# Kernel tuning notes

Measured on AMD Instinct MI355X. Metric: run time of the kernel, lower is better.

Reference implementation:

```python
import jax, jax.numpy as jnp
import numpy as np

N = 2048      # nodes per graph
Q = 9         # output_dim (emotion nodes)
D = 256       # input_dim == hidden_dim
L = 4         # num_layers - 1 GIN layers
B = 32        # batch
E = 32768     # edges per graph
EPS = 1e-5    # BatchNorm eps


def _bn(x, g, b, m, v):
    # eval-mode BatchNorm1d over last (channel) dim
    return (x - m) * (g * jax.lax.rsqrt(v + EPS)) + b


def setup_inputs() -> dict:
    key = jax.random.key(0)
    ks = jax.random.split(key, 18)
    s = 1.0 / np.sqrt(D)
    return {
        "batch_feature": jax.random.normal(ks[0], (B, N, D), jnp.float32),
        "edge_mat": jax.random.randint(ks[1], (2, E), 0, N, dtype=jnp.int32),
        "emotion_emb": jax.random.normal(ks[2], (1, Q, D), jnp.float32) * 0.05,
        "mlp_w1": jax.random.normal(ks[3], (L, D, D), jnp.float32) * s,
        "mlp_b1": jnp.zeros((L, D), jnp.float32),
        "mlp_bn_g": jnp.ones((L, D), jnp.float32),
        "mlp_bn_b": jnp.zeros((L, D), jnp.float32),
        "mlp_bn_m": jax.random.normal(ks[4], (L, D), jnp.float32) * 0.1,
        "mlp_bn_v": jax.random.uniform(ks[5], (L, D), jnp.float32, 0.5, 1.5),
        "mlp_w2": jax.random.normal(ks[6], (L, D, D), jnp.float32) * s,
        "mlp_b2": jnp.zeros((L, D), jnp.float32),
        "bn_g": jnp.ones((L, D), jnp.float32),
        "bn_b": jnp.zeros((L, D), jnp.float32),
        "bn_m": jax.random.normal(ks[7], (L, D), jnp.float32) * 0.1,
        "bn_v": jax.random.uniform(ks[8], (L, D), jnp.float32, 0.5, 1.5),
        "pred_w": jax.random.normal(ks[9], (L + 1, D), jnp.float32) * s,
        "pred_b": jnp.zeros((L + 1,), jnp.float32),
    }


def reference(batch_feature, edge_mat, emotion_emb, mlp_w1, mlp_b1,
              mlp_bn_g, mlp_bn_b, mlp_bn_m, mlp_bn_v, mlp_w2, mlp_b2,
              bn_g, bn_b, bn_m, bn_v, pred_w, pred_b):
    # overwrite first Q node rows with shared emotion embeddings
    h = batch_feature.at[:, :Q, :].set(emotion_emb)          # [B, N, D]
    src, dst = edge_mat[0], edge_mat[1]

    def spmm(x):
        # Adj @ x with self-loops; graph topology shared across batch.
        gathered = x[:, dst, :]                              # [B, E, D]
        agg = jax.vmap(
            lambda g: jax.ops.segment_sum(g, src, num_segments=N)
        )(gathered)                                          # [B, N, D]
        return agg + x  # self-loop (identity added to adjacency)

    hidden = [h]
    for l in range(L):
        pooled = spmm(h)
        # 2-layer GIN MLP: Linear -> BN -> ReLU -> Linear
        t = jnp.einsum('bnd,de->bne', pooled, mlp_w1[l]) + mlp_b1[l]
        t = jax.nn.relu(_bn(t, mlp_bn_g[l], mlp_bn_b[l], mlp_bn_m[l], mlp_bn_v[l]))
        t = jnp.einsum('bnd,de->bne', t, mlp_w2[l]) + mlp_b2[l]
        # outer BatchNorm + ReLU
        h = jax.nn.relu(_bn(t, bn_g[l], bn_b[l], bn_m[l], bn_v[l]))
        hidden.append(h)

    score = jnp.zeros((B, Q), jnp.float32)
    for l, hl in enumerate(hidden):
        h_emotion = hl[:, :Q, :]                             # [B, Q, D]
        score = score + jnp.einsum('bqd,d->bq', h_emotion, pred_w[l]) + pred_b[l]
    return jax.nn.sigmoid(score)                             # [B, Q]
```

## Files before the change

### kernel.cpp

```cpp
#include <hip/hip_runtime.h>
#include <hip/hip_bf16.h>

#define NN 2048
#define QQ 9
#define DD 256
#define LL 4
#define BB 32
#define EE 32768
#define EPSV 1e-5f

typedef __attribute__((ext_vector_type(8))) short bf16x8;
typedef __attribute__((ext_vector_type(8))) ushort u16x8;
typedef __attribute__((ext_vector_type(4))) float f32x4;
typedef __attribute__((ext_vector_type(4))) int i32x4;

__device__ __forceinline__ ushort f2bf(float x)
{
    uint u = __float_as_uint(x);
    u += 0x7FFFu + ((u >> 16) & 1u);
    return (ushort)(u >> 16);
}
__device__ __forceinline__ float bf2f(ushort h)
{
    return __uint_as_float(((uint)h) << 16);
}

__device__ __forceinline__ void gload16(const ushort* g, ushort* l)
{
    __builtin_amdgcn_global_load_lds(
        (const __attribute__((address_space(1))) void*)g,
        (__attribute__((address_space(3))) void*)l, 16, 0, 0);
}

__global__ void k_count(const int* __restrict__ src, int* __restrict__ cnt)
{
    int e = blockIdx.x * blockDim.x + threadIdx.x;
    if (e < EE) atomicAdd(&cnt[src[e]], 1);
}

__global__ __launch_bounds__(256) void k_scan(const int* __restrict__ cnt,
                                              int* __restrict__ row_ptr,
                                              int* __restrict__ cursor)
{
    __shared__ int part[256];
    int t = threadIdx.x;
    int local[8];
    int s = 0;
    #pragma unroll
    for (int i = 0; i < 8; ++i) { local[i] = cnt[t * 8 + i]; s += local[i]; }
    part[t] = s;
    __syncthreads();
    for (int off = 1; off < 256; off <<= 1) {
        int v = (t >= off) ? part[t - off] : 0;
        __syncthreads();
        part[t] += v;
        __syncthreads();
    }
    int run = part[t] - s;
    #pragma unroll
    for (int i = 0; i < 8; ++i) {
        int idx = t * 8 + i;
        row_ptr[idx] = run;
        cursor[idx]  = run;
        run += local[i];
    }
    if (t == 255) row_ptr[NN] = run;
}

__global__ void k_fill(const int* __restrict__ src, const int* __restrict__ dst,
                       int* __restrict__ cursor, int* __restrict__ col)
{
    int e = blockIdx.x * blockDim.x + threadIdx.x;
    if (e < EE) {
        int p = atomicAdd(&cursor[src[e]], 1);
        col[p] = dst[e];
    }
}

__global__ void k_prep0(const float4* __restrict__ bf, const float4* __restrict__ emo,
                        ushort4* __restrict__ hhi)
{
    int total = BB * NN * (DD / 4);
    for (int idx = blockIdx.x * blockDim.x + threadIdx.x; idx < total;
         idx += gridDim.x * blockDim.x) {
        int d4 = idx & 63;
        int n  = (idx >> 6) & (NN - 1);
        float4 v = (n < QQ) ? emo[n * 64 + d4] : bf[idx];
        ushort4 h;
        h.x = f2bf(v.x); h.y = f2bf(v.y); h.z = f2bf(v.z); h.w = f2bf(v.w);
        hhi[idx] = h;
    }
}

__global__ __launch_bounds__(256) void k_spmm6(
    const ushort* __restrict__ phi,
    const int* __restrict__ row_ptr, const int* __restrict__ col,
    ushort* __restrict__ ohi)
{
    int x     = blockIdx.x & 7;
    int local = blockIdx.x >> 3;
    int w     = threadIdx.x >> 6;
    int t     = threadIdx.x & 63;
    int inst  = local * 4 + w;
    int pl    = inst >> 11;
    int n     = inst & (NN - 1);
    int b     = x * 4 + pl * 2 + (t >> 5);
    int q     = t & 31;
    const ushort* base = phi + (size_t)b * NN * DD + q * 8;

    u16x8 sv = *(const u16x8*)(base + (size_t)n * DD);
    float a[8];
    #pragma unroll
    for (int k = 0; k < 8; ++k) a[k] = bf2f((ushort)sv[k]);

    int beg = row_ptr[n], end = row_ptr[n + 1];
    int j = beg;
    for (; j < end && (j & 3); ++j) {
        u16x8 g = *(const u16x8*)(base + (size_t)col[j] * DD);
        #pragma unroll
        for (int k = 0; k < 8; ++k) a[k] += bf2f((ushort)g[k]);
    }
    for (; j + 8 <= end; j += 8) {
        i32x4 c0 = *(const i32x4*)(col + j);
        i32x4 c1 = *(const i32x4*)(col + j + 4);
        u16x8 g[8];
        g[0] = *(const u16x8*)(base + (size_t)c0.x * DD);
        g[1] = *(const u16x8*)(base + (size_t)c0.y * DD);
        g[2] = *(const u16x8*)(base + (size_t)c0.z * DD);
        g[3] = *(const u16x8*)(base + (size_t)c0.w * DD);
        g[4] = *(const u16x8*)(base + (size_t)c1.x * DD);
        g[5] = *(const u16x8*)(base + (size_t)c1.y * DD);
        g[6] = *(const u16x8*)(base + (size_t)c1.z * DD);
        g[7] = *(const u16x8*)(base + (size_t)c1.w * DD);
        #pragma unroll
        for (int u = 0; u < 8; ++u)
            #pragma unroll
            for (int k = 0; k < 8; ++k) a[k] += bf2f((ushort)g[u][k]);
    }
    if (j + 4 <= end) {
        i32x4 c = *(const i32x4*)(col + j);
        u16x8 g[4];
        g[0] = *(const u16x8*)(base + (size_t)c.x * DD);
        g[1] = *(const u16x8*)(base + (size_t)c.y * DD);
        g[2] = *(const u16x8*)(base + (size_t)c.z * DD);
        g[3] = *(const u16x8*)(base + (size_t)c.w * DD);
        #pragma unroll
        for (int u = 0; u < 4; ++u)
            #pragma unroll
            for (int k = 0; k < 8; ++k) a[k] += bf2f((ushort)g[u][k]);
        j += 4;
    }
    for (; j < end; ++j) {
        u16x8 g = *(const u16x8*)(base + (size_t)col[j] * DD);
        #pragma unroll
        for (int k = 0; k < 8; ++k) a[k] += bf2f((ushort)g[k]);
    }

    u16x8 o;
    #pragma unroll
    for (int k = 0; k < 8; ++k) o[k] = f2bf(a[k]);
    *(u16x8*)(ohi + ((size_t)b * NN + n) * DD + q * 8) = o;
}

__global__ __launch_bounds__(256) void k_wprep(const float* __restrict__ w1,
                                               const float* __restrict__ w2,
                                               ushort* __restrict__ wt_hi)
{
    __shared__ float tile[32][36];
    int bx = blockIdx.x;
    int mat = bx >> 6;
    int tt  = bx & 63;
    int tk = (tt >> 3) * 32;
    int tn = (tt & 7) * 32;
    const float* src = (mat < 4) ? (w1 + (size_t)mat * DD * DD)
                                 : (w2 + (size_t)(mat - 4) * DD * DD);
    int t = threadIdx.x;
    int r = t >> 3, c0 = (t & 7) * 4;
    float4 v = *(const float4*)(src + (size_t)(tk + r) * DD + tn + c0);
    tile[r][c0 + 0] = v.x; tile[r][c0 + 1] = v.y;
    tile[r][c0 + 2] = v.z; tile[r][c0 + 3] = v.w;
    __syncthreads();
    int nn = t >> 3, kq = (t & 7) * 4;
    ushort4 hh;
    hh.x = f2bf(tile[kq + 0][nn]); hh.y = f2bf(tile[kq + 1][nn]);
    hh.z = f2bf(tile[kq + 2][nn]); hh.w = f2bf(tile[kq + 3][nn]);
    size_t off = (size_t)mat * DD * DD + (size_t)(tn + nn) * DD + tk + kq;
    *(ushort4*)(wt_hi + off) = hh;
}

__global__ __launch_bounds__(256) void k_gemm_fused(
    const ushort* __restrict__ A, const ushort* __restrict__ W1t,
    const ushort* __restrict__ W2t,
    const float* __restrict__ b1, const float* __restrict__ g1,
    const float* __restrict__ be1, const float* __restrict__ m1,
    const float* __restrict__ v1,
    const float* __restrict__ b2, const float* __restrict__ g2,
    const float* __restrict__ be2, const float* __restrict__ m2,
    const float* __restrict__ v2,
    const float* __restrict__ pw, const float* __restrict__ pb, int l,
    ushort* __restrict__ O, float* __restrict__ out)
{
    __shared__ alignas(16) ushort As[2][64 * 32];
    __shared__ alignas(16) ushort Ws[2][256 * 32];
    __shared__ alignas(16) ushort Ts[64][264];

    int tid = threadIdx.x;
    int x  = blockIdx.x & 7;
    int lm = blockIdx.x >> 3;
    int m0 = x * 8192 + lm * 64;
    int lane = tid & 63;
    int w = tid >> 6;
    int wm = w & 1, wn = w >> 1;
    int lr = lane & 15, kg = lane >> 4;
    int rg = lane >> 4;
    int kgp = kg ^ ((lr >> 1) & 3);

    int sc   = (lane & 3) ^ ((lane >> 3) & 3);
    int srow = lane >> 2;
    const ushort* Aglob = A + (size_t)(m0 + w * 16 + srow) * DD + sc * 8;

    f32x4 acc[2][8];
    #pragma unroll
    for (int m = 0; m < 2; ++m)
        #pragma unroll
        for (int n = 0; n < 8; ++n) acc[m][n] = (f32x4)0.f;

    const ushort* Wg1 = W1t + (size_t)((0 * 4 + w) * 16 + srow) * DD + sc * 8;
    {
        gload16(Aglob, &As[0][w * 512]);
        #pragma unroll
        for (int i = 0; i < 4; ++i) {
            int seg = i * 4 + w;
            gload16(W1t + (size_t)(seg * 16 + srow) * DD + sc * 8, &Ws[0][seg * 512]);
        }
    }
    int cur = 0;
    for (int kc = 0; kc < 8; ++kc) {
        __syncthreads();
        if (kc < 7) {
            int ko = (kc + 1) * 32;
            gload16(Aglob + ko, &As[cur ^ 1][w * 512]);
            #pragma unroll
            for (int i = 0; i < 4; ++i) {
                int seg = i * 4 + w;
                gload16(W1t + (size_t)(seg * 16 + srow) * DD + ko + sc * 8,
                        &Ws[cur ^ 1][seg * 512]);
            }
        }
        bf16x8 ah[2], bh[8];
        #pragma unroll
        for (int mi = 0; mi < 2; ++mi)
            ah[mi] = *(const bf16x8*)&As[cur][(wm * 32 + mi * 16 + lr) * 32 + kgp * 8];
        #pragma unroll
        for (int n = 0; n < 8; ++n)
            bh[n] = *(const bf16x8*)&Ws[cur][(wn * 128 + n * 16 + lr) * 32 + kgp * 8];
        #pragma unroll
        for (int mi = 0; mi < 2; ++mi)
            #pragma unroll
            for (int n = 0; n < 8; ++n)
                acc[mi][n] = __builtin_amdgcn_mfma_f32_16x16x32_bf16(
                    ah[mi], bh[n], acc[mi][n], 0, 0, 0);
        cur ^= 1;
    }
    {
        float sN[8], svN[8];
        #pragma unroll
        for (int n = 0; n < 8; ++n) {
            int jj = wn * 128 + n * 16 + lr;
            sN[n]  = g1[jj] * rsqrtf(v1[jj] + EPSV);
            svN[n] = (b1[jj] - m1[jj]) * sN[n] + be1[jj];
        }
        #pragma unroll
        for (int m = 0; m < 2; ++m)
            #pragma unroll
            for (int n = 0; n < 8; ++n) {
                int cc = wn * 128 + n * 16 + lr;
                #pragma unroll
                for (int r = 0; r < 4; ++r) {
                    float y = acc[m][n][r] * sN[n] + svN[n];
                    Ts[wm * 32 + m * 16 + rg * 4 + r][cc] = f2bf(y > 0.f ? y : 0.f);
                }
            }
    }
    #pragma unroll
    for (int m = 0; m < 2; ++m)
        #pragma unroll
        for (int n = 0; n < 8; ++n) acc[m][n] = (f32x4)0.f;

    {
        #pragma unroll
        for (int i = 0; i < 4; ++i) {
            int seg = i * 4 + w;
            gload16(W2t + (size_t)(seg * 16 + srow) * DD + sc * 8, &Ws[0][seg * 512]);
        }
    }
    cur = 0;
    for (int kc = 0; kc < 8; ++kc) {
        __syncthreads();
        if (kc < 7) {
            int ko = (kc + 1) * 32;
            #pragma unroll
            for (int i = 0; i < 4; ++i) {
                int seg = i * 4 + w;
                gload16(W2t + (size_t)(seg * 16 + srow) * DD + ko + sc * 8,
                        &Ws[cur ^ 1][seg * 512]);
            }
        }
        bf16x8 a2[2], bh[8];
        #pragma unroll
        for (int mi = 0; mi < 2; ++mi)
            a2[mi] = *(const bf16x8*)&Ts[wm * 32 + mi * 16 + lr][kc * 32 + kg * 8];
        #pragma unroll
        for (int n = 0; n < 8; ++n)
            bh[n] = *(const bf16x8*)&Ws[cur][(wn * 128 + n * 16 + lr) * 32 + kgp * 8];
        #pragma unroll
        for (int mi = 0; mi < 2; ++mi)
            #pragma unroll
            for (int n = 0; n < 8; ++n)
                acc[mi][n] = __builtin_amdgcn_mfma_f32_16x16x32_bf16(
                    a2[mi], bh[n], acc[mi][n], 0, 0, 0);
        cur ^= 1;
    }
    __syncthreads();

    {
        float sN[8], svN[8];
        #pragma unroll
        for (int n = 0; n < 8; ++n) {
            int jj = wn * 128 + n * 16 + lr;
            sN[n]  = g2[jj] * rsqrtf(v2[jj] + EPSV);
            svN[n] = (b2[jj] - m2[jj]) * sN[n] + be2[jj];
        }
        #pragma unroll
        for (int m = 0; m < 2; ++m)
            #pragma unroll
            for (int n = 0; n < 8; ++n) {
                int cc = wn * 128 + n * 16 + lr;
                #pragma unroll
                for (int r = 0; r < 4; ++r) {
                    float y = acc[m][n][r] * sN[n] + svN[n];
                    Ts[wm * 32 + m * 16 + rg * 4 + r][cc] = f2bf(y > 0.f ? y : 0.f);
                }
            }
        #pragma unroll
        for (int i = 0; i < 8; ++i) {
            int cid = lane + i * 64;
            int row = cid >> 4, c8 = cid & 15;
            u16x8 vv = *(const u16x8*)&Ts[wm * 32 + row][wn * 128 + c8 * 8];
            *(u16x8*)(O + (size_t)(m0 + wm * 32 + row) * DD + wn * 128 + c8 * 8) = vv;
        }
    }

    __syncthreads();
    if ((m0 & (NN - 1)) == 0) {
        int b = m0 >> 11;
        for (int q = w; q < QQ; q += 4) {
            ushort4 hv = *(const ushort4*)&Ts[q][lane * 4];
            const float4 wv = *(const float4*)&pw[(l + 1) * DD + lane * 4];
            float s = bf2f(hv.x) * wv.x + bf2f(hv.y) * wv.y +
                      bf2f(hv.z) * wv.z + bf2f(hv.w) * wv.w;
            #pragma unroll
            for (int off = 32; off > 0; off >>= 1) s += __shfl_down(s, off);
            if (lane == 0) {
                float v = out[b * QQ + q] + s + pb[l + 1];
                out[b * QQ + q] = (l == LL - 1) ? 1.f / (1.f + expf(-v)) : v;
            }
        }
    }
}

__global__ __launch_bounds__(64) void k_score0(const float4* __restrict__ emo,
                                               const float4* __restrict__ pw,
                                               const float* __restrict__ pb,
                                               float* __restrict__ out)
{
    int q = blockIdx.x, t = threadIdx.x;
    float4 e = emo[q * 64 + t], wv = pw[t];
    float s = e.x * wv.x + e.y * wv.y + e.z * wv.z + e.w * wv.w;
    #pragma unroll
    for (int off = 32; off > 0; off >>= 1) s += __shfl_down(s, off);
    if (t == 0) {
        s += pb[0];
        for (int b = 0; b < BB; ++b) out[b * QQ + q] = s;
    }
}

extern "C" void kernel_launch(void* const* d_in, const int* in_sizes, int n_in,
                              void* d_out, int out_size, void* d_ws, size_t ws_size,
                              hipStream_t stream)
{
    const float* batch = (const float*)d_in[0];
    const int*   edges = (const int*)d_in[1];
    const float* emo   = (const float*)d_in[2];
    const float* w1    = (const float*)d_in[3];
    const float* b1    = (const float*)d_in[4];
    const float* m_g   = (const float*)d_in[5];
    const float* m_b   = (const float*)d_in[6];
    const float* m_m   = (const float*)d_in[7];
    const float* m_v   = (const float*)d_in[8];
    const float* w2    = (const float*)d_in[9];
    const float* b2    = (const float*)d_in[10];
    const float* g_g   = (const float*)d_in[11];
    const float* g_b   = (const float*)d_in[12];
    const float* g_m   = (const float*)d_in[13];
    const float* g_v   = (const float*)d_in[14];
    const float* pw    = (const float*)d_in[15];
    const float* pb    = (const float*)d_in[16];
    float* out = (float*)d_out;

    const size_t HSZ = (size_t)BB * NN * DD;
    const size_t WT  = (size_t)8 * DD * DD;

    ushort* h_hi = (ushort*)d_ws;
    ushort* P_hi = h_hi + HSZ;
    ushort* wt_hi = P_hi + HSZ;
    int* cnt     = (int*)(wt_hi + WT);
    int* row_ptr = cnt + NN;
    int* cursor  = row_ptr + (NN + 4);
    int* col     = cursor + NN;

    const int* src = edges;
    const int* dst = edges + EE;

    hipMemsetAsync(cnt, 0, NN * sizeof(int), stream);
    k_count<<<EE / 256, 256, 0, stream>>>(src, cnt);
    k_scan<<<1, 256, 0, stream>>>(cnt, row_ptr, cursor);
    k_fill<<<EE / 256, 256, 0, stream>>>(src, dst, cursor, col);
    k_wprep<<<512, 256, 0, stream>>>(w1, w2, wt_hi);
    k_prep0<<<4096, 256, 0, stream>>>((const float4*)batch, (const float4*)emo,
                                      (ushort4*)h_hi);
    k_score0<<<QQ, 64, 0, stream>>>((const float4*)emo, (const float4*)pw, pb, out);

    for (int l = 0; l < LL; ++l) {
        k_spmm6<<<8192, 256, 0, stream>>>(h_hi, row_ptr, col, P_hi);
        k_gemm_fused<<<1024, 256, 0, stream>>>(
            P_hi,
            wt_hi + (size_t)l * DD * DD, wt_hi + (size_t)(4 + l) * DD * DD,
            b1 + l * DD, m_g + l * DD, m_b + l * DD, m_m + l * DD, m_v + l * DD,
            b2 + l * DD, g_g + l * DD, g_b + l * DD, g_m + l * DD, g_v + l * DD,
            pw, pb, l,
            h_hi, out);
    }
}
```

Before: 311.9 us.

## Fuse SpMM aggregation into per-layer GEMM kernel with ping-pong hidden buffers

Measured after the change: 373.9 us. 19.9% more time.

```diff
diff --git a/kernel.cpp b/kernel.cpp
--- a/kernel.cpp
+++ b/kernel.cpp
@@ -90,76 +90,6 @@
         h.x = f2bf(v.x); h.y = f2bf(v.y); h.z = f2bf(v.z); h.w = f2bf(v.w);
         hhi[idx] = h;
     }
-}
-
-__global__ __launch_bounds__(256) void k_spmm6(
-    const ushort* __restrict__ phi,
-    const int* __restrict__ row_ptr, const int* __restrict__ col,
-    ushort* __restrict__ ohi)
-{
-    int x     = blockIdx.x & 7;
-    int local = blockIdx.x >> 3;
-    int w     = threadIdx.x >> 6;
-    int t     = threadIdx.x & 63;
-    int inst  = local * 4 + w;
-    int pl    = inst >> 11;
-    int n     = inst & (NN - 1);
-    int b     = x * 4 + pl * 2 + (t >> 5);
-    int q     = t & 31;
-    const ushort* base = phi + (size_t)b * NN * DD + q * 8;
-
-    u16x8 sv = *(const u16x8*)(base + (size_t)n * DD);
-    float a[8];
-    #pragma unroll
-    for (int k = 0; k < 8; ++k) a[k] = bf2f((ushort)sv[k]);
-
-    int beg = row_ptr[n], end = row_ptr[n + 1];
-    int j = beg;
-    for (; j < end && (j & 3); ++j) {
-        u16x8 g = *(const u16x8*)(base + (size_t)col[j] * DD);
-        #pragma unroll
-        for (int k = 0; k < 8; ++k) a[k] += bf2f((ushort)g[k]);
-    }
-    for (; j + 8 <= end; j += 8) {
-        i32x4 c0 = *(const i32x4*)(col + j);
-        i32x4 c1 = *(const i32x4*)(col + j + 4);
-        u16x8 g[8];
-        g[0] = *(const u16x8*)(base + (size_t)c0.x * DD);
-        g[1] = *(const u16x8*)(base + (size_t)c0.y * DD);
-        g[2] = *(const u16x8*)(base + (size_t)c0.z * DD);
-        g[3] = *(const u16x8*)(base + (size_t)c0.w * DD);
-        g[4] = *(const u16x8*)(base + (size_t)c1.x * DD);
-        g[5] = *(const u16x8*)(base + (size_t)c1.y * DD);
-        g[6] = *(const u16x8*)(base + (size_t)c1.z * DD);
-        g[7] = *(const u16x8*)(base + (size_t)c1.w * DD);
-        #pragma unroll
-        for (int u = 0; u < 8; ++u)
-            #pragma unroll
-            for (int k = 0; k < 8; ++k) a[k] += bf2f((ushort)g[u][k]);
-    }
-    if (j + 4 <= end) {
-        i32x4 c = *(const i32x4*)(col + j);
-        u16x8 g[4];
-        g[0] = *(const u16x8*)(base + (size_t)c.x * DD);
-        g[1] = *(const u16x8*)(base + (size_t)c.y * DD);
-        g[2] = *(const u16x8*)(base + (size_t)c.z * DD);
-        g[3] = *(const u16x8*)(base + (size_t)c.w * DD);
-        #pragma unroll
-        for (int u = 0; u < 4; ++u)
-            #pragma unroll
-            for (int k = 0; k < 8; ++k) a[k] += bf2f((ushort)g[u][k]);
-        j += 4;
-    }
-    for (; j < end; ++j) {
-        u16x8 g = *(const u16x8*)(base + (size_t)col[j] * DD);
-        #pragma unroll
-        for (int k = 0; k < 8; ++k) a[k] += bf2f((ushort)g[k]);
-    }
-
-    u16x8 o;
-    #pragma unroll
-    for (int k = 0; k < 8; ++k) o[k] = f2bf(a[k]);
-    *(u16x8*)(ohi + ((size_t)b * NN + n) * DD + q * 8) = o;
 }
 
 __global__ __launch_bounds__(256) void k_wprep(const float* __restrict__ w1,
@@ -188,9 +118,10 @@
     *(ushort4*)(wt_hi + off) = hh;
 }
 
-__global__ __launch_bounds__(256) void k_gemm_fused(
-    const ushort* __restrict__ A, const ushort* __restrict__ W1t,
-    const ushort* __restrict__ W2t,
+__global__ __launch_bounds__(256) void k_layer(
+    const ushort* __restrict__ H, const int* __restrict__ row_ptr,
+    const int* __restrict__ col,
+    const ushort* __restrict__ W1t, const ushort* __restrict__ W2t,
     const float* __restrict__ b1, const float* __restrict__ g1,
     const float* __restrict__ be1, const float* __restrict__ m1,
     const float* __restrict__ v1,
@@ -200,7 +131,6 @@
     const float* __restrict__ pw, const float* __restrict__ pb, int l,
     ushort* __restrict__ O, float* __restrict__ out)
 {
-    __shared__ alignas(16) ushort As[2][64 * 32];
     __shared__ alignas(16) ushort Ws[2][256 * 32];
     __shared__ alignas(16) ushort Ts[64][264];
 
@@ -208,6 +138,8 @@
     int x  = blockIdx.x & 7;
     int lm = blockIdx.x >> 3;
     int m0 = x * 8192 + lm * 64;
+    int b  = m0 >> 11;
+    int n0 = m0 & (NN - 1);
     int lane = tid & 63;
     int w = tid >> 6;
     int wm = w & 1, wn = w >> 1;
@@ -217,7 +149,72 @@
 
     int sc   = (lane & 3) ^ ((lane >> 3) & 3);
     int srow = lane >> 2;
-    const ushort* Aglob = A + (size_t)(m0 + w * 16 + srow) * DD + sc * 8;
+
+    #pragma unroll
+    for (int i = 0; i < 4; ++i) {
+        int seg = i * 4 + w;
+        gload16(W1t + (size_t)(seg * 16 + srow) * DD + sc * 8, &Ws[0][seg * 512]);
+    }
+
+    {
+        int half = lane >> 5;
+        int q    = lane & 31;
+        const ushort* base = H + (size_t)b * NN * DD + q * 8;
+        for (int p = w; p < 32; p += 4) {
+            int row = 2 * p + half;
+            int n   = n0 + row;
+            u16x8 sv = *(const u16x8*)(base + (size_t)n * DD);
+            float a[8];
+            #pragma unroll
+            for (int k = 0; k < 8; ++k) a[k] = bf2f((ushort)sv[k]);
+            int beg = row_ptr[n], end = row_ptr[n + 1];
+            int j = beg;
+            for (; j < end && (j & 3); ++j) {
+                u16x8 g = *(const u16x8*)(base + (size_t)col[j] * DD);
+                #pragma unroll
+                for (int k = 0; k < 8; ++k) a[k] += bf2f((ushort)g[k]);
+            }
+            for (; j + 8 <= end; j += 8) {
+                i32x4 c0 = *(const i32x4*)(col + j);
+                i32x4 c1 = *(const i32x4*)(col + j + 4);
+                u16x8 g[8];
+                g[0] = *(const u16x8*)(base + (size_t)c0.x * DD);
+                g[1] = *(const u16x8*)(base + (size_t)c0.y * DD);
+                g[2] = *(const u16x8*)(base + (size_t)c0.z * DD);
+                g[3] = *(const u16x8*)(base + (size_t)c0.w * DD);
+                g[4] = *(const u16x8*)(base + (size_t)c1.x * DD);
+                g[5] = *(const u16x8*)(base + (size_t)c1.y * DD);
+                g[6] = *(const u16x8*)(base + (size_t)c1.z * DD);
+                g[7] = *(const u16x8*)(base + (size_t)c1.w * DD);
+                #pragma unroll
+                for (int u = 0; u < 8; ++u)
+                    #pragma unroll
+                    for (int k = 0; k < 8; ++k) a[k] += bf2f((ushort)g[u][k]);
+            }
+            if (j + 4 <= end) {
+                i32x4 c = *(const i32x4*)(col + j);
+                u16x8 g[4];
+                g[0] = *(const u16x8*)(base + (size_t)c.x * DD);
+                g[1] = *(const u16x8*)(base + (size_t)c.y * DD);
+                g[2] = *(const u16x8*)(base + (size_t)c.z * DD);
+                g[3] = *(const u16x8*)(base + (size_t)c.w * DD);
+                #pragma unroll
+                for (int u = 0; u < 4; ++u)
+                    #pragma unroll
+                    for (int k = 0; k < 8; ++k) a[k] += bf2f((ushort)g[u][k]);
+                j += 4;
+            }
+            for (; j < end; ++j) {
+                u16x8 g = *(const u16x8*)(base + (size_t)col[j] * DD);
+                #pragma unroll
+                for (int k = 0; k < 8; ++k) a[k] += bf2f((ushort)g[k]);
+            }
+            u16x8 o;
+            #pragma unroll
+            for (int k = 0; k < 8; ++k) o[k] = f2bf(a[k]);
+            *(u16x8*)&Ts[row][q * 8] = o;
+        }
+    }
 
     f32x4 acc[2][8];
     #pragma unroll
@@ -225,21 +222,12 @@
         #pragma unroll
         for (int n = 0; n < 8; ++n) acc[m][n] = (f32x4)0.f;
 
-    const ushort* Wg1 = W1t + (size_t)((0 * 4 + w) * 16 + srow) * DD + sc * 8;
-    {
-        gload16(Aglob, &As[0][w * 512]);
-        #pragma unroll
-        for (int i = 0; i < 4; ++i) {
-            int seg = i * 4 + w;
-            gload16(W1t + (size_t)(seg * 16 + srow) * DD + sc * 8, &Ws[0][seg * 512]);
-        }
-    }
+    __syncthreads();
     int cur = 0;
     for (int kc = 0; kc < 8; ++kc) {
-        __syncthreads();
+        if (kc > 0) __syncthreads();
         if (kc < 7) {
             int ko = (kc + 1) * 32;
-            gload16(Aglob + ko, &As[cur ^ 1][w * 512]);
             #pragma unroll
             for (int i = 0; i < 4; ++i) {
                 int seg = i * 4 + w;
@@ -250,7 +238,7 @@
         bf16x8 ah[2], bh[8];
         #pragma unroll
         for (int mi = 0; mi < 2; ++mi)
-            ah[mi] = *(const bf16x8*)&As[cur][(wm * 32 + mi * 16 + lr) * 32 + kgp * 8];
+            ah[mi] = *(const bf16x8*)&Ts[wm * 32 + mi * 16 + lr][kc * 32 + kg * 8];
         #pragma unroll
         for (int n = 0; n < 8; ++n)
             bh[n] = *(const bf16x8*)&Ws[cur][(wn * 128 + n * 16 + lr) * 32 + kgp * 8];
@@ -262,6 +250,14 @@
                     ah[mi], bh[n], acc[mi][n], 0, 0, 0);
         cur ^= 1;
     }
+    __syncthreads();
+
+    #pragma unroll
+    for (int i = 0; i < 4; ++i) {
+        int seg = i * 4 + w;
+        gload16(W2t + (size_t)(seg * 16 + srow) * DD + sc * 8, &Ws[0][seg * 512]);
+    }
+
     {
         float sN[8], svN[8];
         #pragma unroll
@@ -287,16 +283,10 @@
         #pragma unroll
         for (int n = 0; n < 8; ++n) acc[m][n] = (f32x4)0.f;
 
-    {
-        #pragma unroll
-        for (int i = 0; i < 4; ++i) {
-            int seg = i * 4 + w;
-            gload16(W2t + (size_t)(seg * 16 + srow) * DD + sc * 8, &Ws[0][seg * 512]);
-        }
-    }
+    __syncthreads();
     cur = 0;
     for (int kc = 0; kc < 8; ++kc) {
-        __syncthreads();
+        if (kc > 0) __syncthreads();
         if (kc < 7) {
             int ko = (kc + 1) * 32;
             #pragma unroll
@@ -352,8 +342,7 @@
     }
 
     __syncthreads();
-    if ((m0 & (NN - 1)) == 0) {
-        int b = m0 >> 11;
+    if (n0 == 0) {
         for (int q = w; q < QQ; q += 4) {
             ushort4 hv = *(const ushort4*)&Ts[q][lane * 4];
             const float4 wv = *(const float4*)&pw[(l + 1) * DD + lane * 4];
@@ -411,9 +400,9 @@
     const size_t HSZ = (size_t)BB * NN * DD;
     const size_t WT  = (size_t)8 * DD * DD;
 
-    ushort* h_hi = (ushort*)d_ws;
-    ushort* P_hi = h_hi + HSZ;
-    ushort* wt_hi = P_hi + HSZ;
+    ushort* H0 = (ushort*)d_ws;
+    ushort* H1 = H0 + HSZ;
+    ushort* wt_hi = H1 + HSZ;
     int* cnt     = (int*)(wt_hi + WT);
     int* row_ptr = cnt + NN;
     int* cursor  = row_ptr + (NN + 4);
@@ -428,17 +417,19 @@
     k_fill<<<EE / 256, 256, 0, stream>>>(src, dst, cursor, col);
     k_wprep<<<512, 256, 0, stream>>>(w1, w2, wt_hi);
     k_prep0<<<4096, 256, 0, stream>>>((const float4*)batch, (const float4*)emo,
-                                      (ushort4*)h_hi);
+                                      (ushort4*)H0);
     k_score0<<<QQ, 64, 0, stream>>>((const float4*)emo, (const float4*)pw, pb, out);
 
+    ushort* hc = H0;
+    ushort* hn = H1;
     for (int l = 0; l < LL; ++l) {
-        k_spmm6<<<8192, 256, 0, stream>>>(h_hi, row_ptr, col, P_hi);
-        k_gemm_fused<<<1024, 256, 0, stream>>>(
-            P_hi,
+        k_layer<<<1024, 256, 0, stream>>>(
+            hc, row_ptr, col,
             wt_hi + (size_t)l * DD * DD, wt_hi + (size_t)(4 + l) * DD * DD,
             b1 + l * DD, m_g + l * DD, m_b + l * DD, m_m + l * DD, m_v + l * DD,
             b2 + l * DD, g_g + l * DD, g_b + l * DD, g_m + l * DD, g_v + l * DD,
             pw, pb, l,
-            h_hi, out);
-    }
-}
+            hn, out);
+        ushort* tmp = hc; hc = hn; hn = tmp;
+    }
+}
```
